# Performance work log

Measured on AMD Instinct MI355X. Metric: run time of the kernel, lower is better.

The kernel has to match this reference:

```python
import jax, jax.numpy as jnp
import numpy as np

B, LA, LQ, LO, H, OUT = 32, 2048, 64, 32, 1024, 5


def _kaiming(key, out_f, in_f):
    return jax.random.normal(key, (out_f, in_f), jnp.float32) * np.sqrt(2.0 / in_f)


def setup_inputs() -> dict:
    key = jax.random.key(0)
    ks = jax.random.split(key, 16)
    inp = {
        "article_contexts": jax.random.normal(ks[0], (B, LA, H), jnp.float32),
        "question_contexts": jax.random.normal(ks[1], (B, LQ, H), jnp.float32),
        "options_embeds": jax.random.normal(ks[2], (B, 5, LO, H), jnp.float32),
        "answer_indices": jax.random.randint(ks[3], (B,), 0, LQ),
    }
    # mlp_att (article-question attention) params
    inp["a_Qw"], inp["a_Qb"] = _kaiming(ks[4], H, H), jnp.zeros((H,), jnp.float32)
    inp["a_Kw"], inp["a_Kb"] = _kaiming(ks[5], H, H), jnp.zeros((H,), jnp.float32)
    inp["a_Vw"], inp["a_Vb"] = _kaiming(ks[6], H, H), jnp.zeros((H,), jnp.float32)
    inp["a_vw"], inp["a_vb"] = _kaiming(ks[7], 1, H), jnp.zeros((1,), jnp.float32)
    # dot_layer (option attention) params
    inp["d_Qw"], inp["d_Qb"] = _kaiming(ks[8], H, H), jnp.zeros((H,), jnp.float32)
    inp["d_Kw"], inp["d_Kb"] = _kaiming(ks[9], H, H), jnp.zeros((H,), jnp.float32)
    inp["d_Vw"], inp["d_Vb"] = _kaiming(ks[10], H, H), jnp.zeros((H,), jnp.float32)
    inp["d_vw"], inp["d_vb"] = _kaiming(ks[11], 1, H), jnp.zeros((1,), jnp.float32)
    # final linear: hidden_size*5 -> output_dim
    inp["f_w"], inp["f_b"] = _kaiming(ks[12], OUT, 5 * H), jnp.zeros((OUT,), jnp.float32)
    return inp


def _mlp_att(Q, K, V, Qw, Qb, Kw, Kb, Vw, Vb, vw, vb):
    # Q: [B, H]; K, V: [B, (..opt..), L, H]. Dropout is identity (eval mode).
    Qp = Q @ Qw.T + Qb                      # [B, H]
    Kp = K @ Kw.T + Kb                      # [..., L, H]
    Vp = V @ Vw.T + Vb                      # [..., L, H]
    while Qp.ndim < Kp.ndim:
        Qp = Qp[..., None, :]
    M = jnp.tanh(Qp + Kp)                   # [..., L, H]
    scores = jax.nn.softmax(M @ vw.T + vb, axis=-2)  # softmax over L, [..., L, 1]
    return jnp.sum(Vp * scores, axis=-2)    # [..., H]


def reference(article_contexts, question_contexts, options_embeds, answer_indices,
              a_Qw, a_Qb, a_Kw, a_Kb, a_Vw, a_Vb, a_vw, a_vb,
              d_Qw, d_Qb, d_Kw, d_Kb, d_Vw, d_Vb, d_vw, d_vb,
              f_w, f_b):
    b = article_contexts.shape[0]
    # gather question context at the answer index -> [B, H]
    oqc = question_contexts[jnp.arange(b), answer_indices]
    # article-question additive attention -> [B, H]
    aq = _mlp_att(oqc, article_contexts, article_contexts,
                  a_Qw, a_Qb, a_Kw, a_Kb, a_Vw, a_Vb, a_vw, a_vb)
    # per-option additive attention, vectorized over the 5 options -> [B, 5, H]
    feats = _mlp_att(aq, options_embeds, options_embeds,
                     d_Qw, d_Qb, d_Kw, d_Kb, d_Vw, d_Vb, d_vw, d_vb)
    # concat options along feature dim, final linear -> [B, OUT]
    logits = feats.reshape(b, -1) @ f_w.T + f_b
    return logits
```

## Files before the change

### kernel.cpp

```cpp
#include <hip/hip_runtime.h>
#include <hip/hip_bf16.h>
#include <math.h>

#define HDIM 1024
#define NB 32
#define LA 2048
#define LO 32

typedef __attribute__((ext_vector_type(8))) short bf16x8;
typedef __attribute__((ext_vector_type(4))) float f32x4;
typedef unsigned int u32;

__device__ __forceinline__ float tanh_fast(float x){
    return 2.0f / (1.0f + __expf(-2.0f * x)) - 1.0f;
}

__device__ __forceinline__ void load_lds16(const void* gptr, void* lptr){
    __builtin_amdgcn_global_load_lds(
        (const __attribute__((address_space(1))) u32*)gptr,
        (__attribute__((address_space(3))) u32*)lptr, 16, 0, 0);
}

__global__ void zero_kernel(float* __restrict__ p, int n){
    int i = blockIdx.x * blockDim.x + threadIdx.x;
    int stride = gridDim.x * blockDim.x;
    for (; i < n; i += stride) p[i] = 0.0f;
}

__global__ void conv_bf16_kernel(const float* __restrict__ in, __hip_bfloat16* __restrict__ out, long n){
    long i = ((long)blockIdx.x * blockDim.x + threadIdx.x) * 4;
    long stride = (long)gridDim.x * blockDim.x * 4;
    for (; i < n; i += stride){
        float4 v = *(const float4*)(in + i);
        union { __hip_bfloat16 h[4]; short4 s; } u;
        u.h[0] = __float2bfloat16(v.x); u.h[1] = __float2bfloat16(v.y);
        u.h[2] = __float2bfloat16(v.z); u.h[3] = __float2bfloat16(v.w);
        *(short4*)(out + i) = u.s;
    }
}

__global__ void gather_kernel(const float* __restrict__ qc, const int* __restrict__ ans,
                              float* __restrict__ oqc){
    int b = blockIdx.x, tid = threadIdx.x;
    int idx = ans[b];
    const float* src = qc + ((size_t)b * 64 + idx) * HDIM;
    float* dst = oqc + (size_t)b * HDIM;
    #pragma unroll
    for (int l = 0; l < 4; l++) dst[tid + l * 256] = src[tid + l * 256];
}

__global__ __launch_bounds__(256) void proj_kernel(
    const float* __restrict__ in, const float* __restrict__ W,
    const float* __restrict__ bias, float* __restrict__ out){
    __shared__ float xin[HDIM];
    const int g = blockIdx.x, tid = threadIdx.x;
    const int lane = tid & 63, wave = tid >> 6;
    *(float4*)&xin[tid * 4] = *(const float4*)&in[(size_t)g * HDIM + tid * 4];
    __syncthreads();
    float4 xv[4];
    #pragma unroll
    for (int c = 0; c < 4; c++) xv[c] = *(const float4*)&xin[(c * 64 + lane) * 4];
    const int hbase = blockIdx.y * 64 + wave * 16;
    #pragma unroll 4
    for (int r = 0; r < 16; r++){
        int h = hbase + r;
        const float* Wr = W + (size_t)h * HDIM;
        float p = 0.f;
        #pragma unroll
        for (int c = 0; c < 4; c++){
            float4 wv = *(const float4*)&Wr[(c * 64 + lane) * 4];
            p = fmaf(xv[c].x, wv.x, p); p = fmaf(xv[c].y, wv.y, p);
            p = fmaf(xv[c].z, wv.z, p); p = fmaf(xv[c].w, wv.w, p);
        }
        #pragma unroll
        for (int off = 1; off < 64; off <<= 1) p += __shfl_xor(p, off, 64);
        if (lane == 0) out[(size_t)g * HDIM + h] = p + bias[h];
    }
}

#define NT 32
__global__ __launch_bounds__(512, 4) void score_mfma_f32b(
    const float* __restrict__ Xf, const __hip_bfloat16* __restrict__ Kw,
    const float* __restrict__ Kb, const float* __restrict__ Qp,
    const float* __restrict__ vw, float* __restrict__ s,
    int rows_per_batch)
{
    __shared__ __align__(16) char lds[49152];
    const int tid = threadIdx.x;
    const int lane = tid & 63, wid = tid >> 6;
    const int wm = wid >> 2, wn = wid & 3;
    const int lr = lane & 15, lg = lane >> 4;

    const int na = gridDim.x >> 3;
    const int bid = blockIdx.x;
    const int xcd = bid & 7, seq = bid >> 3;
    const int a_idx = xcd * (na >> 3) + (seq >> 3);
    const int h_idx = seq & 7;
    const int a0 = a_idx * 256, h0 = h_idx * 128;

    f32x4 acc[4][4] = {};

    const int rA = tid >> 2;
    const int srcbA = ((tid & 3) * 16) ^ (((rA >> 1) & 3) << 4);
    const char* pA = (const char*)Kw + (size_t)(h0 + rA) * 2048 + srcbA;
    char* dA = lds + tid * 16;

    const int rB = tid >> 1;
    const int hb = tid & 1;
    const float* pB = Xf + (size_t)(a0 + rB) * HDIM + hb * 16;
    const int swzB = ((rB >> 1) & 3) << 4;
    char* dB0 = lds + 8192 + rB * 64 + ((hb * 32) ^ swzB);
    char* dB1 = lds + 8192 + rB * 64 + ((hb * 32 + 16) ^ swzB);

    int aoff[4], boff[4];
    #pragma unroll
    for (int hf = 0; hf < 4; hf++){
        int rw = wm * 64 + hf * 16 + lr;
        aoff[hf] = rw * 64 + ((lg * 16) ^ (((rw >> 1) & 3) << 4));
    }
    #pragma unroll
    for (int af = 0; af < 4; af++){
        int rw = wn * 64 + af * 16 + lr;
        boff[af] = 8192 + rw * 64 + ((lg * 16) ^ (((rw >> 1) & 3) << 4));
    }

    float4 br0, br1, br2, br3;
#define LOADB(kt) do { const float* q = pB + (kt) * 32; \
    br0 = *(const float4*)q; br1 = *(const float4*)(q + 4); \
    br2 = *(const float4*)(q + 8); br3 = *(const float4*)(q + 12); } while(0)
#define CVTWRITE(bufoff) do { \
    union { __hip_bfloat16 h[8]; bf16x8 v; } u0, u1; \
    u0.h[0]=__float2bfloat16(br0.x); u0.h[1]=__float2bfloat16(br0.y); \
    u0.h[2]=__float2bfloat16(br0.z); u0.h[3]=__float2bfloat16(br0.w); \
    u0.h[4]=__float2bfloat16(br1.x); u0.h[5]=__float2bfloat16(br1.y); \
    u0.h[6]=__float2bfloat16(br1.z); u0.h[7]=__float2bfloat16(br1.w); \
    u1.h[0]=__float2bfloat16(br2.x); u1.h[1]=__float2bfloat16(br2.y); \
    u1.h[2]=__float2bfloat16(br2.z); u1.h[3]=__float2bfloat16(br2.w); \
    u1.h[4]=__float2bfloat16(br3.x); u1.h[5]=__float2bfloat16(br3.y); \
    u1.h[6]=__float2bfloat16(br3.z); u1.h[7]=__float2bfloat16(br3.w); \
    *(bf16x8*)(dB0 + (bufoff)) = u0.v; \
    *(bf16x8*)(dB1 + (bufoff)) = u1.v; } while(0)
#define ISSUEA(kt, bufoff) load_lds16(pA + (size_t)(kt) * 64, dA + (bufoff))
#define COMPUTE(bufoff) do { \
    bf16x8 av[4], bv[4]; \
    _Pragma("unroll") \
    for (int hf = 0; hf < 4; hf++) av[hf] = *(const bf16x8*)(lds + (bufoff) + aoff[hf]); \
    _Pragma("unroll") \
    for (int af = 0; af < 4; af++) bv[af] = *(const bf16x8*)(lds + (bufoff) + boff[af]); \
    __builtin_amdgcn_s_setprio(1); \
    _Pragma("unroll") \
    for (int hf = 0; hf < 4; hf++) \
        _Pragma("unroll") \
        for (int af = 0; af < 4; af++) \
            acc[hf][af] = __builtin_amdgcn_mfma_f32_16x16x32_bf16(av[hf], bv[af], acc[hf][af], 0, 0, 0); \
    __builtin_amdgcn_s_setprio(0); } while(0)

    ISSUEA(0, 0);
    LOADB(0);
    CVTWRITE(0);
    asm volatile("s_waitcnt vmcnt(0)" ::: "memory");
    __syncthreads();

    int bo = 0;
    for (int t = 0; t < NT; ++t){
        if (t < NT - 1){
            ISSUEA(t + 1, bo ^ 24576);
            LOADB(t + 1);
        }
        COMPUTE(bo);
        if (t < NT - 1){
            CVTWRITE(bo ^ 24576);
            asm volatile("s_waitcnt vmcnt(0)" ::: "memory");
        }
        __syncthreads();
        bo ^= 24576;
    }

    const int b = a0 / rows_per_batch;
    float qv[4][4], vv[4][4];
    #pragma unroll
    for (int hf = 0; hf < 4; hf++){
        int hbase = h0 + wm * 64 + hf * 16 + lg * 4;
        float4 kb4 = *(const float4*)(Kb + hbase);
        float4 qp4 = *(const float4*)(Qp + (size_t)b * HDIM + hbase);
        float4 vw4 = *(const float4*)(vw + hbase);
        qv[hf][0] = kb4.x + qp4.x; qv[hf][1] = kb4.y + qp4.y;
        qv[hf][2] = kb4.z + qp4.z; qv[hf][3] = kb4.w + qp4.w;
        vv[hf][0] = vw4.x; vv[hf][1] = vw4.y; vv[hf][2] = vw4.z; vv[hf][3] = vw4.w;
    }
    #pragma unroll
    for (int af = 0; af < 4; af++){
        float sacc = 0.f;
        #pragma unroll
        for (int hf = 0; hf < 4; hf++)
            #pragma unroll
            for (int r = 0; r < 4; r++)
                sacc += tanh_fast(acc[hf][af][r] + qv[hf][r]) * vv[hf][r];
        sacc += __shfl_xor(sacc, 16, 64);
        sacc += __shfl_xor(sacc, 32, 64);
        if (lane < 16)
            atomicAdd(&s[a0 + wn * 64 + af * 16 + lr], sacc);
    }
#undef LOADB
#undef CVTWRITE
#undef ISSUEA
#undef COMPUTE
}

#define SBM 128
#define SBN 128
__global__ __launch_bounds__(256) void score_mfma_kernel(
    const __hip_bfloat16* __restrict__ X, const __hip_bfloat16* __restrict__ Kw,
    const float* __restrict__ Kb, const float* __restrict__ Qp,
    const float* __restrict__ vw, float* __restrict__ s,
    int row_off, int rows_per_batch)
{
    __shared__ __align__(16) __hip_bfloat16 As[SBM][32];
    __shared__ __align__(16) __hip_bfloat16 Bs[SBN][32];
    const int tid = threadIdx.x;
    const int lane = tid & 63, wid = tid >> 6;
    const int wm = wid >> 1, wn = wid & 1;
    const int row0 = blockIdx.x * SBM;
    const int h0 = blockIdx.y * SBN;
    const int lr = lane & 15, lg = lane >> 4;

    f32x4 acc[4][4] = {};

    for (int k0 = 0; k0 < HDIM; k0 += 32){
        #pragma unroll
        for (int l = 0; l < 2; l++){
            int f = tid + l * 256;
            int r = f >> 2, c8 = (f & 3) * 8;
            load_lds16(X + (size_t)(row0 + r) * HDIM + k0 + c8, &As[0][0] + f * 8);
            load_lds16(Kw + (size_t)(h0 + r) * HDIM + k0 + c8, &Bs[0][0] + f * 8);
        }
        __syncthreads();
        bf16x8 a[4], b[4];
        #pragma unroll
        for (int i = 0; i < 4; i++)
            a[i] = *(const bf16x8*)&As[wm * 64 + i * 16 + lr][lg * 8];
        #pragma unroll
        for (int j = 0; j < 4; j++)
            b[j] = *(const bf16x8*)&Bs[wn * 64 + j * 16 + lr][lg * 8];
        #pragma unroll
        for (int i = 0; i < 4; i++)
            #pragma unroll
            for (int j = 0; j < 4; j++)
                acc[i][j] = __builtin_amdgcn_mfma_f32_16x16x32_bf16(a[i], b[j], acc[i][j], 0, 0, 0);
        __syncthreads();
    }

    float kbv[4], vwv[4];
    #pragma unroll
    for (int j = 0; j < 4; j++){
        int h = h0 + wn * 64 + j * 16 + lr;
        kbv[j] = Kb[h]; vwv[j] = vw[h];
    }
    #pragma unroll
    for (int i = 0; i < 4; i++){
        #pragma unroll
        for (int reg = 0; reg < 4; reg++){
            int r = row0 + wm * 64 + i * 16 + lg * 4 + reg;
            int gr = row_off + r;
            int bb = gr / rows_per_batch;
            const float* Qpb = Qp + (size_t)bb * HDIM;
            float p = 0.f;
            #pragma unroll
            for (int j = 0; j < 4; j++){
                int h = h0 + wn * 64 + j * 16 + lr;
                p += tanh_fast(acc[i][j][reg] + kbv[j] + Qpb[h]) * vwv[j];
            }
            #pragma unroll
            for (int off = 1; off < 16; off <<= 1) p += __shfl_xor(p, off, 16);
            if (lr == 0) atomicAdd(&s[gr], p);
        }
    }
}

__global__ void softmax_kernel(float* __restrict__ s, int Rg){
    __shared__ float red[4];
    int g = blockIdx.x, tid = threadIdx.x;
    float* sg = s + (size_t)g * Rg;
    float m = -INFINITY;
    for (int i = tid; i < Rg; i += 256) m = fmaxf(m, sg[i]);
    #pragma unroll
    for (int off = 32; off > 0; off >>= 1) m = fmaxf(m, __shfl_down(m, off, 64));
    if ((tid & 63) == 0) red[tid >> 6] = m;
    __syncthreads();
    m = fmaxf(fmaxf(red[0], red[1]), fmaxf(red[2], red[3]));
    __syncthreads();
    float sum = 0.f;
    for (int i = tid; i < Rg; i += 256){ float e = __expf(sg[i] - m); sg[i] = e; sum += e; }
    #pragma unroll
    for (int off = 32; off > 0; off >>= 1) sum += __shfl_down(sum, off, 64);
    if ((tid & 63) == 0) red[tid >> 6] = sum;
    __syncthreads();
    float inv = 1.0f / (red[0] + red[1] + red[2] + red[3]);
    for (int i = tid; i < Rg; i += 256) sg[i] *= inv;
}

__global__ void wsum_kernel(const float* __restrict__ X, const float* __restrict__ sc,
                            float* __restrict__ out, int Rg, int rowsPerChunk){
    __shared__ float scs[256];
    int g = blockIdx.x >> 2;
    int kc = blockIdx.x & 3;
    int i0 = blockIdx.y * rowsPerChunk;
    int tid = threadIdx.x;
    if (tid < rowsPerChunk) scs[tid] = sc[(size_t)g * Rg + i0 + tid];
    __syncthreads();
    int k = kc * 256 + tid;
    const float* Xg = X + ((size_t)g * Rg + i0) * HDIM + k;
    float acc = 0.f;
    for (int i = 0; i < rowsPerChunk; i++)
        acc += scs[i] * Xg[(size_t)i * HDIM];
    atomicAdd(&out[(size_t)g * HDIM + k], acc);
}

__global__ void final_kernel(const float* __restrict__ feats, const float* __restrict__ fw,
                             const float* __restrict__ fb, float* __restrict__ out){
    __shared__ float red[4];
    int b = blockIdx.x, tid = threadIdx.x;
    const float* fe = feats + (size_t)b * 5120;
    for (int j = 0; j < 5; j++){
        float acc = 0.f;
        for (int i = tid; i < 5120; i += 256) acc += fe[i] * fw[(size_t)j * 5120 + i];
        #pragma unroll
        for (int off = 32; off > 0; off >>= 1) acc += __shfl_down(acc, off, 64);
        if ((tid & 63) == 0) red[tid >> 6] = acc;
        __syncthreads();
        if (tid == 0) out[b * 5 + j] = fb[j] + red[0] + red[1] + red[2] + red[3];
        __syncthreads();
    }
}

extern "C" void kernel_launch(void* const* d_in, const int* in_sizes, int n_in,
                              void* d_out, int out_size, void* d_ws, size_t ws_size,
                              hipStream_t stream) {
    const float* article  = (const float*)d_in[0];
    const float* question = (const float*)d_in[1];
    const float* options  = (const float*)d_in[2];
    const int*   ans      = (const int*)d_in[3];
    const float* a_Qw = (const float*)d_in[4];  const float* a_Qb = (const float*)d_in[5];
    const float* a_Kw = (const float*)d_in[6];  const float* a_Kb = (const float*)d_in[7];
    const float* a_Vw = (const float*)d_in[8];  const float* a_Vb = (const float*)d_in[9];
    const float* a_vw = (const float*)d_in[10];
    const float* d_Qw = (const float*)d_in[12]; const float* d_Qb = (const float*)d_in[13];
    const float* d_Kw = (const float*)d_in[14]; const float* d_Kb = (const float*)d_in[15];
    const float* d_Vw = (const float*)d_in[16]; const float* d_Vb = (const float*)d_in[17];
    const float* d_vw = (const float*)d_in[18];
    const float* f_w  = (const float*)d_in[20]; const float* f_b  = (const float*)d_in[21];
    float* out = (float*)d_out;

    float* ws = (float*)d_ws;
    float* oqc   = ws;
    float* qp_a  = ws + 32768;
    float* aq    = ws + 65536;
    float* qp_d  = ws + 98304;
    float* feats = ws + 131072;
    float* s_art = ws + 294912;
    float* s_opt = ws + 360448;
    float* w_art = ws + 365568;
    float* wd    = ws + 398336;
    __hip_bfloat16* kwa_bf = (__hip_bfloat16*)(ws + 562176);
    __hip_bfloat16* kwd_bf = kwa_bf + 1048576;
    __hip_bfloat16* opt_bf = kwd_bf + 1048576;

    zero_kernel<<<256, 256, 0, stream>>>(s_art, 267264);
    gather_kernel<<<NB, 256, 0, stream>>>(question, ans, oqc);
    proj_kernel<<<dim3(NB, 16), 256, 0, stream>>>(oqc, a_Qw, a_Qb, qp_a);
    conv_bf16_kernel<<<64, 256, 0, stream>>>(a_Kw, kwa_bf, 1048576);

    score_mfma_f32b<<<(NB * LA / 256) * 8, 512, 0, stream>>>(
        article, kwa_bf, a_Kb, qp_a, a_vw, s_art, LA);
    softmax_kernel<<<NB, 256, 0, stream>>>(s_art, LA);
    wsum_kernel<<<dim3(NB * 4, 8), 256, 0, stream>>>(article, s_art, w_art, LA, 256);
    proj_kernel<<<dim3(NB, 16), 256, 0, stream>>>(w_art, a_Vw, a_Vb, aq);

    proj_kernel<<<dim3(NB, 16), 256, 0, stream>>>(aq, d_Qw, d_Qb, qp_d);
    conv_bf16_kernel<<<64, 256, 0, stream>>>(d_Kw, kwd_bf, 1048576);
    conv_bf16_kernel<<<320, 256, 0, stream>>>(options, opt_bf, 5242880);
    score_mfma_kernel<<<dim3((NB * 5 * LO) / SBM, HDIM / SBN), 256, 0, stream>>>(
        opt_bf, kwd_bf, d_Kb, qp_d, d_vw, s_opt, 0, 5 * LO);
    softmax_kernel<<<NB * 5, 256, 0, stream>>>(s_opt, LO);
    wsum_kernel<<<dim3(NB * 5 * 4, 1), 256, 0, stream>>>(options, s_opt, wd, LO, LO);
    proj_kernel<<<dim3(NB * 5, 16), 256, 0, stream>>>(wd, d_Vw, d_Vb, feats);
    final_kernel<<<NB, 256, 0, stream>>>(feats, f_w, f_b, out);
}
```

Measured before the change: 490.0 us.

## Stream fp32 article tiles directly to LDS and convert to bf16 at fragment load

The article-score GEMM now copies fp32 article rows straight into LDS with global_load_lds, instead of staging them through registers and converting to bf16 before the LDS write. The bf16 conversion moves into the compute step, right after the fragment read. The M tile is halved to 128 rows so the fp32 tile fits the same LDS budget, and the grid doubles to match. The loop becomes a two-deep prefetch pipeline using partial vmcnt waits and raw barriers, meant to overlap global loads with MFMA. In exchange it adds per-step conversion ALU work, halves MFMA reuse per A fragment, and doubles the atomic adds into the score buffer.

```diff
diff --git a/kernel.cpp b/kernel.cpp
--- a/kernel.cpp
+++ b/kernel.cpp
@@ -79,7 +79,7 @@
 }
 
 #define NT 32
-__global__ __launch_bounds__(512, 4) void score_mfma_f32b(
+__global__ __launch_bounds__(512, 4) void score_f32b(
     const float* __restrict__ Xf, const __hip_bfloat16* __restrict__ Kw,
     const float* __restrict__ Kb, const float* __restrict__ Qp,
     const float* __restrict__ vw, float* __restrict__ s,
@@ -96,85 +96,80 @@
     const int xcd = bid & 7, seq = bid >> 3;
     const int a_idx = xcd * (na >> 3) + (seq >> 3);
     const int h_idx = seq & 7;
-    const int a0 = a_idx * 256, h0 = h_idx * 128;
-
-    f32x4 acc[4][4] = {};
+    const int a0 = a_idx * 128, h0 = h_idx * 128;
+
+    f32x4 acc[4][2] = {};
 
     const int rA = tid >> 2;
     const int srcbA = ((tid & 3) * 16) ^ (((rA >> 1) & 3) << 4);
     const char* pA = (const char*)Kw + (size_t)(h0 + rA) * 2048 + srcbA;
     char* dA = lds + tid * 16;
 
-    const int rB = tid >> 1;
-    const int hb = tid & 1;
-    const float* pB = Xf + (size_t)(a0 + rB) * HDIM + hb * 16;
-    const int swzB = ((rB >> 1) & 3) << 4;
-    char* dB0 = lds + 8192 + rB * 64 + ((hb * 32) ^ swzB);
-    char* dB1 = lds + 8192 + rB * 64 + ((hb * 32 + 16) ^ swzB);
-
-    int aoff[4], boff[4];
+    const int rho0 = tid >> 3, s0 = tid & 7;
+    const int sigB = (s0 ^ (rho0 & 7)) * 16;
+    const char* pB0 = (const char*)Xf + (size_t)(a0 + rho0) * 4096 + sigB;
+    const char* pB1 = (const char*)Xf + (size_t)(a0 + rho0 + 64) * 4096 + sigB;
+    char* dB0 = lds + 8192 + tid * 16;
+    char* dB1 = lds + 16384 + tid * 16;
+
+    int aoff[4];
     #pragma unroll
     for (int hf = 0; hf < 4; hf++){
         int rw = wm * 64 + hf * 16 + lr;
         aoff[hf] = rw * 64 + ((lg * 16) ^ (((rw >> 1) & 3) << 4));
     }
-    #pragma unroll
-    for (int af = 0; af < 4; af++){
-        int rw = wn * 64 + af * 16 + lr;
-        boff[af] = 8192 + rw * 64 + ((lg * 16) ^ (((rw >> 1) & 3) << 4));
-    }
-
-    float4 br0, br1, br2, br3;
-#define LOADB(kt) do { const float* q = pB + (kt) * 32; \
-    br0 = *(const float4*)q; br1 = *(const float4*)(q + 4); \
-    br2 = *(const float4*)(q + 8); br3 = *(const float4*)(q + 12); } while(0)
-#define CVTWRITE(bufoff) do { \
-    union { __hip_bfloat16 h[8]; bf16x8 v; } u0, u1; \
-    u0.h[0]=__float2bfloat16(br0.x); u0.h[1]=__float2bfloat16(br0.y); \
-    u0.h[2]=__float2bfloat16(br0.z); u0.h[3]=__float2bfloat16(br0.w); \
-    u0.h[4]=__float2bfloat16(br1.x); u0.h[5]=__float2bfloat16(br1.y); \
-    u0.h[6]=__float2bfloat16(br1.z); u0.h[7]=__float2bfloat16(br1.w); \
-    u1.h[0]=__float2bfloat16(br2.x); u1.h[1]=__float2bfloat16(br2.y); \
-    u1.h[2]=__float2bfloat16(br2.z); u1.h[3]=__float2bfloat16(br2.w); \
-    u1.h[4]=__float2bfloat16(br3.x); u1.h[5]=__float2bfloat16(br3.y); \
-    u1.h[6]=__float2bfloat16(br3.z); u1.h[7]=__float2bfloat16(br3.w); \
-    *(bf16x8*)(dB0 + (bufoff)) = u0.v; \
-    *(bf16x8*)(dB1 + (bufoff)) = u1.v; } while(0)
-#define ISSUEA(kt, bufoff) load_lds16(pA + (size_t)(kt) * 64, dA + (bufoff))
+    int boff[2][2];
+    #pragma unroll
+    for (int af = 0; af < 2; af++){
+        int rho = wn * 32 + af * 16 + lr;
+        boff[af][0] = 8192 + rho * 128 + (((2 * lg)     ^ (rho & 7)) * 16);
+        boff[af][1] = 8192 + rho * 128 + (((2 * lg + 1) ^ (rho & 7)) * 16);
+    }
+
+#define STAGE(kt, bufoff) do { \
+    load_lds16(pA  + (size_t)(kt) * 64,  dA  + (bufoff)); \
+    load_lds16(pB0 + (size_t)(kt) * 128, dB0 + (bufoff)); \
+    load_lds16(pB1 + (size_t)(kt) * 128, dB1 + (bufoff)); } while(0)
+
 #define COMPUTE(bufoff) do { \
-    bf16x8 av[4], bv[4]; \
+    bf16x8 av[4], bv[2]; \
     _Pragma("unroll") \
     for (int hf = 0; hf < 4; hf++) av[hf] = *(const bf16x8*)(lds + (bufoff) + aoff[hf]); \
     _Pragma("unroll") \
-    for (int af = 0; af < 4; af++) bv[af] = *(const bf16x8*)(lds + (bufoff) + boff[af]); \
+    for (int af = 0; af < 2; af++){ \
+        f32x4 x0 = *(const f32x4*)(lds + (bufoff) + boff[af][0]); \
+        f32x4 x1 = *(const f32x4*)(lds + (bufoff) + boff[af][1]); \
+        union { __hip_bfloat16 h[8]; bf16x8 v; } u; \
+        u.h[0] = __float2bfloat16(x0[0]); u.h[1] = __float2bfloat16(x0[1]); \
+        u.h[2] = __float2bfloat16(x0[2]); u.h[3] = __float2bfloat16(x0[3]); \
+        u.h[4] = __float2bfloat16(x1[0]); u.h[5] = __float2bfloat16(x1[1]); \
+        u.h[6] = __float2bfloat16(x1[2]); u.h[7] = __float2bfloat16(x1[3]); \
+        bv[af] = u.v; \
+    } \
     __builtin_amdgcn_s_setprio(1); \
     _Pragma("unroll") \
     for (int hf = 0; hf < 4; hf++) \
         _Pragma("unroll") \
-        for (int af = 0; af < 4; af++) \
+        for (int af = 0; af < 2; af++) \
             acc[hf][af] = __builtin_amdgcn_mfma_f32_16x16x32_bf16(av[hf], bv[af], acc[hf][af], 0, 0, 0); \
     __builtin_amdgcn_s_setprio(0); } while(0)
 
-    ISSUEA(0, 0);
-    LOADB(0);
-    CVTWRITE(0);
+    STAGE(0, 0);
+    STAGE(1, 24576);
+    int bo = 0;
+    for (int kt = 0; kt < NT - 1; ++kt){
+        asm volatile("s_waitcnt vmcnt(3)" ::: "memory");
+        __builtin_amdgcn_s_barrier();
+        __builtin_amdgcn_sched_barrier(0);
+        COMPUTE(bo);
+        __builtin_amdgcn_s_barrier();
+        if (kt < NT - 2) STAGE(kt + 2, bo);
+        bo ^= 24576;
+    }
     asm volatile("s_waitcnt vmcnt(0)" ::: "memory");
-    __syncthreads();
-
-    int bo = 0;
-    for (int t = 0; t < NT; ++t){
-        if (t < NT - 1){
-            ISSUEA(t + 1, bo ^ 24576);
-            LOADB(t + 1);
-        }
-        COMPUTE(bo);
-        if (t < NT - 1){
-            CVTWRITE(bo ^ 24576);
-            asm volatile("s_waitcnt vmcnt(0)" ::: "memory");
-        }
-        __syncthreads();
-        bo ^= 24576;
-    }
+    __builtin_amdgcn_s_barrier();
+    __builtin_amdgcn_sched_barrier(0);
+    COMPUTE(bo);
 
     const int b = a0 / rows_per_batch;
     float qv[4][4], vv[4][4];
@@ -189,7 +184,7 @@
         vv[hf][0] = vw4.x; vv[hf][1] = vw4.y; vv[hf][2] = vw4.z; vv[hf][3] = vw4.w;
     }
     #pragma unroll
-    for (int af = 0; af < 4; af++){
+    for (int af = 0; af < 2; af++){
         float sacc = 0.f;
         #pragma unroll
         for (int hf = 0; hf < 4; hf++)
@@ -199,11 +194,9 @@
         sacc += __shfl_xor(sacc, 16, 64);
         sacc += __shfl_xor(sacc, 32, 64);
         if (lane < 16)
-            atomicAdd(&s[a0 + wn * 64 + af * 16 + lr], sacc);
-    }
-#undef LOADB
-#undef CVTWRITE
-#undef ISSUEA
+            atomicAdd(&s[a0 + wn * 32 + af * 16 + lr], sacc);
+    }
+#undef STAGE
 #undef COMPUTE
 }
 
@@ -370,7 +363,7 @@
     proj_kernel<<<dim3(NB, 16), 256, 0, stream>>>(oqc, a_Qw, a_Qb, qp_a);
     conv_bf16_kernel<<<64, 256, 0, stream>>>(a_Kw, kwa_bf, 1048576);
 
-    score_mfma_f32b<<<(NB * LA / 256) * 8, 512, 0, stream>>>(
+    score_f32b<<<(NB * LA / 128) * 8, 512, 0, stream>>>(
         article, kwa_bf, a_Kb, qp_a, a_vw, s_art, LA);
     softmax_kernel<<<NB, 256, 0, stream>>>(s_art, LA);
     wsum_kernel<<<dim3(NB * 4, 8), 256, 0, stream>>>(article, s_art, w_art, LA, 256);
```

Result: faster. 471.1 us (-3.9%).
